# Kernel tuning notes

Measured on AMD Instinct MI355X. Metric: run time of the kernel, lower is better.

Reference implementation:

```python
import jax, jax.numpy as jnp
import numpy as np

B, T, S, H = 32, 512, 1024, 512


def setup_inputs() -> dict:
    key = jax.random.key(0)
    k1, k2, k3, k4, k5, k6 = jax.random.split(key, 6)
    scale = 1.0 / np.sqrt(H)
    return {
        "query": jax.random.normal(k1, (B, T, H), dtype=jnp.float32),
        "encoder_outputs": jax.random.normal(k2, (B, S, H), dtype=jnp.float32),
        "src_lengths": jax.random.randint(k3, (B,), 1, S + 1, dtype=jnp.int32),
        "Ws": jax.random.normal(k4, (H, H), dtype=jnp.float32) * scale,  # torch Linear weight [out,in]
        "Wh": jax.random.normal(k5, (H, H), dtype=jnp.float32) * scale,
        "v": jax.random.normal(k6, (H,), dtype=jnp.float32) * scale,
    }


def reference(query, encoder_outputs, src_lengths, Ws, Wh, v):
    # score(h_s, q_t) = v^T tanh(Wh h_s + Ws q_t); masked softmax over src; weighted sum.
    S_ = encoder_outputs.shape[1]
    # Wh(encoder_outputs) computed once (loop in original recomputes it each step; same math).
    Whe = jnp.einsum('bsh,oh->bso', encoder_outputs, Wh)  # [B,S,H]
    mask = jnp.arange(S_)[None, :] < src_lengths[:, None]  # [B,S] valid positions

    def step(carry, q_t):  # q_t: [B,H]
        Wsq = jnp.einsum('bh,oh->bo', q_t, Ws)            # [B,H]
        scores = jnp.einsum('bsh,h->bs', jnp.tanh(Whe + Wsq[:, None, :]), v)  # [B,S]
        scores = jnp.where(mask, scores, -jnp.inf)
        attn = jax.nn.softmax(scores, axis=-1)            # [B,S]
        ctx = jnp.einsum('bs,bsh->bh', attn, encoder_outputs)  # [B,H]
        return carry, (ctx, attn)

    _, (ctx_t, attn_t) = jax.lax.scan(step, None, jnp.swapaxes(query, 0, 1))
    context_vectors = jnp.swapaxes(ctx_t, 0, 1)  # [B,T,H]
    # original returns attention weights from the LAST timestep only
    return context_vectors, attn_t[-1]
```

## Files before the change

kernel.cpp:

```cpp
#include <hip/hip_runtime.h>


constexpr int B = 32, T = 512, S = 1024, H = 512;
constexpr int TT = 16;
constexpr int SP = S + 8;
constexpr float C2LOG2E = 2.88539008177792681f;

typedef float vf4 __attribute__((ext_vector_type(4)));
typedef float f32x4 __attribute__((ext_vector_type(4)));
typedef short bf16x8 __attribute__((ext_vector_type(8)));
typedef unsigned short ushort_t;

#define DEVI __device__ __forceinline__

DEVI unsigned pack_bf16(float a, float b) {
  unsigned ua = __builtin_bit_cast(unsigned, a) + 0x8000u;
  unsigned ub = __builtin_bit_cast(unsigned, b) + 0x8000u;
  return (ub & 0xffff0000u) | (ua >> 16);
}
DEVI ushort_t to_bf16u(float x) {
  return (ushort_t)((__builtin_bit_cast(unsigned, x) + 0x8000u) >> 16);
}
DEVI float bf_lo(unsigned d) { return __builtin_bit_cast(float, d << 16); }
DEVI float bf_hi(unsigned d) { return __builtin_bit_cast(float, d & 0xffff0000u); }
DEVI float bf_one(ushort_t u) { return __builtin_bit_cast(float, (unsigned)u << 16); }
DEVI float exp2c(float x) {
  return __builtin_amdgcn_exp2f(fminf(fmaxf(x, -15.f), 15.f));
}

constexpr int QBLK = (B * T / 128) * 4;
constexpr int EBLK = (B * S / 128) * 4;

__global__ __launch_bounds__(256)
void mfma_matmul_kernel(const float* __restrict__ query, const float* __restrict__ enc,
                        const float* __restrict__ Ws, const float* __restrict__ Wh,
                        float* __restrict__ q4, float* __restrict__ e4,
                        const int* __restrict__ lens) {
  __shared__ short As[128][72];
  __shared__ short Bs[128][72];
  const int tid = threadIdx.x;
  int blk = blockIdx.x;
  const bool isE = blk >= QBLK;
  if (isE) blk -= QBLK;
  const int bx = blk & 3, by = blk >> 2;
  const int row0 = by * 128, col0 = bx * 128;
  const float* A = isE ? enc : query;
  const float* W = isE ? Wh : Ws;
  if (isE && (row0 % S) >= lens[row0 / S]) return;

  const int lr = tid >> 4;
  const int lc = (tid & 15) * 4;
  const int lane = tid & 63, wv = tid >> 6;
  const int wm = (wv >> 1) * 64, wn = (wv & 1) * 64;
  const int lrow = lane & 15, lkg = (lane >> 4) * 8;

  f32x4 acc[4][4] = {};
  for (int k0 = 0; k0 < H; k0 += 64) {
    __syncthreads();
#pragma unroll
    for (int u = 0; u < 8; ++u) {
      int r = lr + u * 16;
      float4 av = *(const float4*)&A[(size_t)(row0 + r) * H + k0 + lc];
      *(uint2*)&As[r][lc] = make_uint2(pack_bf16(av.x, av.y), pack_bf16(av.z, av.w));
      float4 wv4 = *(const float4*)&W[(size_t)(col0 + r) * H + k0 + lc];
      *(uint2*)&Bs[r][lc] = make_uint2(pack_bf16(wv4.x, wv4.y), pack_bf16(wv4.z, wv4.w));
    }
    __syncthreads();
#pragma unroll
    for (int ks = 0; ks < 64; ks += 32) {
      bf16x8 af[4], bfr[4];
#pragma unroll
      for (int i = 0; i < 4; ++i) {
        af[i] = *(const bf16x8*)&As[wm + i * 16 + lrow][ks + lkg];
        bfr[i] = *(const bf16x8*)&Bs[wn + i * 16 + lrow][ks + lkg];
      }
#pragma unroll
      for (int mt = 0; mt < 4; ++mt)
#pragma unroll
        for (int nt = 0; nt < 4; ++nt)
          acc[mt][nt] = __builtin_amdgcn_mfma_f32_16x16x32_bf16(
              af[mt], bfr[nt], acc[mt][nt], 0, 0, 0);
    }
  }

  const int crow = (lane >> 4) * 4, ccol = lane & 15;
  if (!isE) {
    const int b = row0 / T;
#pragma unroll
    for (int mt = 0; mt < 4; ++mt) {
      const int m = (row0 % T) + wm + mt * 16 + crow;
      const int tile_t = m >> 2;
#pragma unroll
      for (int nt = 0; nt < 4; ++nt) {
        const int n = col0 + wn + nt * 16 + ccol;
        float* base = q4 + (size_t)b * T * H + (size_t)tile_t * (4 * H) +
                      (n >> 2) * 16 + (n & 3);
        f32x4 a = acc[mt][nt];
#pragma unroll
        for (int reg = 0; reg < 4; ++reg) base[reg * 4] = exp2c(C2LOG2E * a[reg]);
      }
    }
  } else {
    const int b = row0 / S;
#pragma unroll
    for (int mt = 0; mt < 4; ++mt) {
      const int s0 = (row0 % S) + wm + mt * 16 + crow;
#pragma unroll
      for (int nt = 0; nt < 4; ++nt) {
        const int n = col0 + wn + nt * 16 + ccol;
        float* base = e4 + (size_t)b * H * S + (size_t)(n >> 2) * (4 * S) +
                      (size_t)s0 * 4 + (n & 3);
        f32x4 a = acc[mt][nt];
#pragma unroll
        for (int reg = 0; reg < 4; ++reg) base[reg * 4] = exp2c(C2LOG2E * a[reg]);
      }
    }
  }
}

DEVI void tree4(float& acc, vf4 q, vf4 vv, vf4 e) {
  float a0 = __builtin_fmaf(q[0], e[0], 1.0f);
  float a1 = __builtin_fmaf(q[1], e[1], 1.0f);
  float a2 = __builtin_fmaf(q[2], e[2], 1.0f);
  float a3 = __builtin_fmaf(q[3], e[3], 1.0f);
  float d01 = a0 * a1, d23 = a2 * a3;
  float n01 = __builtin_fmaf(vv[1], a0, vv[0] * a1);
  float n23 = __builtin_fmaf(vv[3], a2, vv[2] * a3);
  float d = d01 * d23;
  float n = __builtin_fmaf(n23, d01, n01 * d23);
  acc = __builtin_fmaf(n, __builtin_amdgcn_rcpf(d), acc);
}

DEVI vf4 qload4(const ushort_t (&s_q4)[32][64], int h4q, int t) {
  uint2 qu = *(const uint2*)&s_q4[h4q][t * 4];
  vf4 q = {bf_lo(qu.x), bf_hi(qu.x), bf_lo(qu.y), bf_hi(qu.y)};
  return q;
}

DEVI void stage_quarter(ushort_t (&s_q4)[32][64], const vf4* __restrict__ qsrc,
                        int qt, int tid) {
  __syncthreads();
#pragma unroll
  for (int u = 0; u < 2; ++u) {
    int g = tid + u * 256;
    int tile = g >> 7, rem = g & 127;
    int h4q = rem >> 2, i = rem & 3;
    vf4 qv = qsrc[tile * 512 + (qt * 32 + h4q) * 4 + i];
    uint2 pk = make_uint2(pack_bf16(qv[0], qv[1]), pack_bf16(qv[2], qv[3]));
    ((uint2*)&s_q4[0][0])[h4q * 16 + tile * 4 + i] = pk;
  }
  __syncthreads();
}

template <int NSIM>
DEVI void passN16(ushort_t (&s_q4)[32][64], const vf4* __restrict__ qsrc,
                  const float* __restrict__ v, const float* __restrict__ e4b,
                  ushort_t (&s_sc16)[TT][SP], int wv, int lane) {
  const int tid = wv * 64 + lane;
  float acc[NSIM][TT];
#pragma unroll
  for (int r = 0; r < NSIM; ++r)
#pragma unroll
    for (int t = 0; t < TT; ++t) acc[r][t] = 0.f;
  const float* ep = e4b + (size_t)(wv * 64 + lane) * 4;
  for (int qt = 0; qt < 4; ++qt) {
    stage_quarter(s_q4, qsrc, qt, tid);
    for (int h4q = 0; h4q < 32; ++h4q) {
      const int h4 = qt * 32 + h4q;
      vf4 e[NSIM];
#pragma unroll
      for (int r = 0; r < NSIM; ++r)
        e[r] = *(const vf4*)(ep + (size_t)h4 * (S * 4) + r * 1024);
      vf4 vv = *(const vf4*)(v + h4 * 4);
#pragma unroll
      for (int t = 0; t < TT; ++t) {
        vf4 q = qload4(s_q4, h4q, t);
#pragma unroll
        for (int r = 0; r < NSIM; ++r) tree4(acc[r][t], q, vv, e[r]);
      }
    }
  }
#pragma unroll
  for (int r = 0; r < NSIM; ++r) {
    const int s = (wv + 4 * r) * 64 + lane;
#pragma unroll
    for (int t = 0; t < TT; ++t) s_sc16[t][s] = to_bf16u(-2.0f * acc[r][t]);
  }
}

template <int R>
DEVI void passTail16(ushort_t (&s_q4)[32][64], const vf4* __restrict__ qsrc,
                     const float* __restrict__ v, const float* __restrict__ e4b,
                     ushort_t (&s_sc16)[TT][SP], int kbase, int wv, int lane) {
  const int tid = wv * 64 + lane;
  float acc[R][4];
#pragma unroll
  for (int r = 0; r < R; ++r)
#pragma unroll
    for (int jj = 0; jj < 4; ++jj) acc[r][jj] = 0.f;
  const float* ep = e4b + (size_t)(kbase * 64 + lane) * 4;
  for (int qt = 0; qt < 4; ++qt) {
    stage_quarter(s_q4, qsrc, qt, tid);
    for (int h4q = 0; h4q < 32; ++h4q) {
      const int h4 = qt * 32 + h4q;
      vf4 vv = *(const vf4*)(v + h4 * 4);
      vf4 e[R];
#pragma unroll
      for (int r = 0; r < R; ++r)
        e[r] = *(const vf4*)(ep + (size_t)h4 * (S * 4) + r * 256);
#pragma unroll
      for (int jj = 0; jj < 4; ++jj) {
        vf4 q = qload4(s_q4, h4q, wv + 4 * jj);
#pragma unroll
        for (int r = 0; r < R; ++r) tree4(acc[r][jj], q, vv, e[r]);
      }
    }
  }
#pragma unroll
  for (int r = 0; r < R; ++r)
#pragma unroll
    for (int jj = 0; jj < 4; ++jj)
      s_sc16[wv + 4 * jj][(kbase + r) * 64 + lane] = to_bf16u(-2.0f * acc[r][jj]);
}

__global__ __launch_bounds__(256, 4)
void attn_fused_kernel(const float* __restrict__ wsq, const float* __restrict__ wheT,
                       const float* __restrict__ enc, const float* __restrict__ v,
                       const int* __restrict__ lens, float* __restrict__ out) {
  __shared__ __align__(16) ushort_t s_sc16[TT][SP];
  __shared__ __align__(16) ushort_t s_q4[32][64];
  __shared__ long long s_w[32];
  __shared__ int s_bsel;

  const int tid = threadIdx.x;
  const int xcd = blockIdx.x & 7;
  const int j = blockIdx.x >> 3;
  const int slot = j >> 5;
  const int tt = j & 31;

  if (tid < 32) s_w[tid] = ((long long)lens[tid] << 8) + tid;
  __syncthreads();
  if (tid < 32) {
    long long wb = s_w[tid];
    int rank = 0;
#pragma unroll
    for (int b2 = 0; b2 < 32; ++b2) rank += (s_w[b2] > wb);
    int myrank = slot * 8 + ((slot & 1) ? (7 - xcd) : xcd);
    if (rank == myrank) s_bsel = tid;
  }
  __syncthreads();
  const int b = __builtin_amdgcn_readfirstlane(s_bsel);
  const int len = lens[b];

  {
    const int wv = tid >> 6, lane = tid & 63;
    const int NS = (len + 63) >> 6;
    const int nsw = NS >> 2;
    const int R = NS & 3;
    const float* e4b = wheT + (size_t)b * H * S;
    const vf4* qsrc = (const vf4*)(wsq + (size_t)b * T * H + (size_t)tt * (TT * H));
    switch (nsw) {
      case 1: passN16<1>(s_q4, qsrc, v, e4b, s_sc16, wv, lane); break;
      case 2: passN16<2>(s_q4, qsrc, v, e4b, s_sc16, wv, lane); break;
      case 3: passN16<3>(s_q4, qsrc, v, e4b, s_sc16, wv, lane); break;
      case 4: passN16<4>(s_q4, qsrc, v, e4b, s_sc16, wv, lane); break;
      default: break;
    }
    switch (R) {
      case 1: passTail16<1>(s_q4, qsrc, v, e4b, s_sc16, nsw * 4, wv, lane); break;
      case 2: passTail16<2>(s_q4, qsrc, v, e4b, s_sc16, nsw * 4, wv, lane); break;
      case 3: passTail16<3>(s_q4, qsrc, v, e4b, s_sc16, nsw * 4, wv, lane); break;
      default: break;
    }
  }
  __syncthreads();

  {
    const int wv = tid >> 6, lane = tid & 63;
#pragma unroll
    for (int jj = 0; jj < 4; ++jj) {
      const int tr = wv + 4 * jj;
      float ps[S / 64];
      float sum = 0.f;
#pragma unroll
      for (int i = 0; i < S / 64; ++i) {
        int s = lane + 64 * i;
        float sc = bf_one(s_sc16[tr][s]);
        float p = (s < len) ? __builtin_amdgcn_exp2f(sc * 1.44269504088896341f) : 0.f;
        ps[i] = p;
        sum += p;
      }
#pragma unroll
      for (int o = 1; o < 64; o <<= 1) sum += __shfl_xor(sum, o, 64);
      float rs = 1.0f / sum;
#pragma unroll
      for (int i = 0; i < S / 64; ++i) {
        float pn = ps[i] * rs;
        s_sc16[tr][lane + 64 * i] = to_bf16u(pn);
        if (tt == T / TT - 1 && tr == TT - 1)
          out[(size_t)B * T * H + (size_t)b * S + lane + 64 * i] = pn;
      }
    }
  }
  __syncthreads();

  {
    const int wv = tid >> 6, lane = tid & 63;
    const int lrow = lane & 15, lkg = (lane >> 4) * 8;
    const int hbase = wv * 128;
    const float* encb = enc + (size_t)b * S * H;
    f32x4 acc[8] = {};
    const int nch = (len + 31) >> 5;
    for (int kc = 0; kc < nch; ++kc) {
      const int k0 = kc * 32 + lkg;
      bf16x8 pa = *(const bf16x8*)&s_sc16[lrow][k0];
#pragma unroll
      for (int nt = 0; nt < 8; ++nt) {
        const int h = hbase + nt * 16 + lrow;
        const float* ep = encb + (size_t)k0 * H + h;
        float b0 = ep[0 * H], b1 = ep[1 * H], b2 = ep[2 * H], b3 = ep[3 * H];
        float b4 = ep[4 * H], b5 = ep[5 * H], b6 = ep[6 * H], b7 = ep[7 * H];
        uint4 uu = make_uint4(pack_bf16(b0, b1), pack_bf16(b2, b3),
                              pack_bf16(b4, b5), pack_bf16(b6, b7));
        bf16x8 bfr = __builtin_bit_cast(bf16x8, uu);
        acc[nt] = __builtin_amdgcn_mfma_f32_16x16x32_bf16(pa, bfr, acc[nt], 0, 0, 0);
      }
    }
    const int crow = (lane >> 4) * 4, ccol = lane & 15;
#pragma unroll
    for (int nt = 0; nt < 8; ++nt) {
      const int h = hbase + nt * 16 + ccol;
#pragma unroll
      for (int reg = 0; reg < 4; ++reg) {
        const int t = crow + reg;
        out[((size_t)b * T + tt * TT + t) * H + h] = acc[nt][reg];
      }
    }
  }
}

extern "C" void kernel_launch(void* const* d_in, const int* in_sizes, int n_in,
                              void* d_out, int out_size, void* d_ws, size_t ws_size,
                              hipStream_t stream) {
  const float* query = (const float*)d_in[0];
  const float* enc   = (const float*)d_in[1];
  const int*   lens  = (const int*)d_in[2];
  const float* Ws    = (const float*)d_in[3];
  const float* Wh    = (const float*)d_in[4];
  const float* v     = (const float*)d_in[5];
  float* out = (float*)d_out;
  float* wsq  = (float*)d_ws;
  float* wheT = wsq + (size_t)B * T * H;

  mfma_matmul_kernel<<<dim3(QBLK + EBLK), 256, 0, stream>>>(query, enc, Ws, Wh, wsq, wheT, lens);
  attn_fused_kernel<<<dim3(B * (T / TT)), 256, 0, stream>>>(wsq, wheT, enc, v, lens, out);
}
```

Before: 496.2 us.

## Merge rational tanh sums over eight hidden dims and cap per-pass S chunks

The rational-form tanh score accumulation now combines eight hidden dimensions per reciprocal instead of four. This halves the rcp count and cuts the accumulator update work per element. The main S pass is split into chunks of at most two sub-tiles per call instead of one call with up to four, which lowers accumulator register pressure but restages Wsq in LDS once per chunk. The -2 scale is folded into the softmax exponent constant. Products of eight denominators risk overflow or precision loss in fp32.

```diff
diff --git a/kernel.cpp b/kernel.cpp
--- a/kernel.cpp
+++ b/kernel.cpp
@@ -118,17 +118,27 @@
   }
 }
 
-DEVI void tree4(float& acc, vf4 q, vf4 vv, vf4 e) {
-  float a0 = __builtin_fmaf(q[0], e[0], 1.0f);
-  float a1 = __builtin_fmaf(q[1], e[1], 1.0f);
-  float a2 = __builtin_fmaf(q[2], e[2], 1.0f);
-  float a3 = __builtin_fmaf(q[3], e[3], 1.0f);
-  float d01 = a0 * a1, d23 = a2 * a3;
-  float n01 = __builtin_fmaf(vv[1], a0, vv[0] * a1);
-  float n23 = __builtin_fmaf(vv[3], a2, vv[2] * a3);
-  float d = d01 * d23;
-  float n = __builtin_fmaf(n23, d01, n01 * d23);
-  acc = __builtin_fmaf(n, __builtin_amdgcn_rcpf(d), acc);
+DEVI void tree8(float& acc, vf4 qa, vf4 qb, vf4 va, vf4 vb, vf4 ea, vf4 eb) {
+  float a0 = __builtin_fmaf(qa[0], ea[0], 1.0f);
+  float a1 = __builtin_fmaf(qa[1], ea[1], 1.0f);
+  float a2 = __builtin_fmaf(qa[2], ea[2], 1.0f);
+  float a3 = __builtin_fmaf(qa[3], ea[3], 1.0f);
+  float b0 = __builtin_fmaf(qb[0], eb[0], 1.0f);
+  float b1 = __builtin_fmaf(qb[1], eb[1], 1.0f);
+  float b2 = __builtin_fmaf(qb[2], eb[2], 1.0f);
+  float b3 = __builtin_fmaf(qb[3], eb[3], 1.0f);
+  float dA01 = a0 * a1, dA23 = a2 * a3;
+  float dB01 = b0 * b1, dB23 = b2 * b3;
+  float nA01 = __builtin_fmaf(va[1], a0, va[0] * a1);
+  float nA23 = __builtin_fmaf(va[3], a2, va[2] * a3);
+  float nB01 = __builtin_fmaf(vb[1], b0, vb[0] * b1);
+  float nB23 = __builtin_fmaf(vb[3], b2, vb[2] * b3);
+  float dA = dA01 * dA23, dB = dB01 * dB23;
+  float nA = __builtin_fmaf(nA23, dA01, nA01 * dA23);
+  float nB = __builtin_fmaf(nB23, dB01, nB01 * dB23);
+  float D = dA * dB;
+  float N = __builtin_fmaf(nA, dB, nB * dA);
+  acc = __builtin_fmaf(N, __builtin_amdgcn_rcpf(D), acc);
 }
 
 DEVI vf4 qload4(const ushort_t (&s_q4)[32][64], int h4q, int t) {
@@ -155,36 +165,41 @@
 template <int NSIM>
 DEVI void passN16(ushort_t (&s_q4)[32][64], const vf4* __restrict__ qsrc,
                   const float* __restrict__ v, const float* __restrict__ e4b,
-                  ushort_t (&s_sc16)[TT][SP], int wv, int lane) {
+                  ushort_t (&s_sc16)[TT][SP], int ks0, int wv, int lane) {
   const int tid = wv * 64 + lane;
   float acc[NSIM][TT];
 #pragma unroll
   for (int r = 0; r < NSIM; ++r)
 #pragma unroll
     for (int t = 0; t < TT; ++t) acc[r][t] = 0.f;
-  const float* ep = e4b + (size_t)(wv * 64 + lane) * 4;
+  const float* ep = e4b + (size_t)(wv * 64 + lane) * 4 + (size_t)ks0 * 1024;
   for (int qt = 0; qt < 4; ++qt) {
     stage_quarter(s_q4, qsrc, qt, tid);
-    for (int h4q = 0; h4q < 32; ++h4q) {
-      const int h4 = qt * 32 + h4q;
-      vf4 e[NSIM];
-#pragma unroll
-      for (int r = 0; r < NSIM; ++r)
-        e[r] = *(const vf4*)(ep + (size_t)h4 * (S * 4) + r * 1024);
-      vf4 vv = *(const vf4*)(v + h4 * 4);
+    for (int g = 0; g < 16; ++g) {
+      const int h4 = qt * 32 + 2 * g;
+      vf4 ea[NSIM], eb[NSIM];
+#pragma unroll
+      for (int r = 0; r < NSIM; ++r) {
+        ea[r] = *(const vf4*)(ep + (size_t)h4 * (S * 4) + r * 1024);
+        eb[r] = *(const vf4*)(ep + (size_t)(h4 + 1) * (S * 4) + r * 1024);
+      }
+      vf4 va = *(const vf4*)(v + h4 * 4);
+      vf4 vb = *(const vf4*)(v + h4 * 4 + 4);
 #pragma unroll
       for (int t = 0; t < TT; ++t) {
-        vf4 q = qload4(s_q4, h4q, t);
-#pragma unroll
-        for (int r = 0; r < NSIM; ++r) tree4(acc[r][t], q, vv, e[r]);
+        vf4 qa = qload4(s_q4, 2 * g, t);
+        vf4 qb = qload4(s_q4, 2 * g + 1, t);
+#pragma unroll
+        for (int r = 0; r < NSIM; ++r)
+          tree8(acc[r][t], qa, qb, va, vb, ea[r], eb[r]);
       }
     }
   }
 #pragma unroll
   for (int r = 0; r < NSIM; ++r) {
-    const int s = (wv + 4 * r) * 64 + lane;
-#pragma unroll
-    for (int t = 0; t < TT; ++t) s_sc16[t][s] = to_bf16u(-2.0f * acc[r][t]);
+    const int s = (wv + 4 * (ks0 + r)) * 64 + lane;
+#pragma unroll
+    for (int t = 0; t < TT; ++t) s_sc16[t][s] = to_bf16u(acc[r][t]);
   }
 }
 
@@ -201,18 +216,23 @@
   const float* ep = e4b + (size_t)(kbase * 64 + lane) * 4;
   for (int qt = 0; qt < 4; ++qt) {
     stage_quarter(s_q4, qsrc, qt, tid);
-    for (int h4q = 0; h4q < 32; ++h4q) {
-      const int h4 = qt * 32 + h4q;
-      vf4 vv = *(const vf4*)(v + h4 * 4);
-      vf4 e[R];
-#pragma unroll
-      for (int r = 0; r < R; ++r)
-        e[r] = *(const vf4*)(ep + (size_t)h4 * (S * 4) + r * 256);
+    for (int g = 0; g < 16; ++g) {
+      const int h4 = qt * 32 + 2 * g;
+      vf4 va = *(const vf4*)(v + h4 * 4);
+      vf4 vb = *(const vf4*)(v + h4 * 4 + 4);
+      vf4 ea[R], eb[R];
+#pragma unroll
+      for (int r = 0; r < R; ++r) {
+        ea[r] = *(const vf4*)(ep + (size_t)h4 * (S * 4) + r * 256);
+        eb[r] = *(const vf4*)(ep + (size_t)(h4 + 1) * (S * 4) + r * 256);
+      }
 #pragma unroll
       for (int jj = 0; jj < 4; ++jj) {
-        vf4 q = qload4(s_q4, h4q, wv + 4 * jj);
-#pragma unroll
-        for (int r = 0; r < R; ++r) tree4(acc[r][jj], q, vv, e[r]);
+        vf4 qa = qload4(s_q4, 2 * g, wv + 4 * jj);
+        vf4 qb = qload4(s_q4, 2 * g + 1, wv + 4 * jj);
+#pragma unroll
+        for (int r = 0; r < R; ++r)
+          tree8(acc[r][jj], qa, qb, va, vb, ea[r], eb[r]);
       }
     }
   }
@@ -220,7 +240,7 @@
   for (int r = 0; r < R; ++r)
 #pragma unroll
     for (int jj = 0; jj < 4; ++jj)
-      s_sc16[wv + 4 * jj][(kbase + r) * 64 + lane] = to_bf16u(-2.0f * acc[r][jj]);
+      s_sc16[wv + 4 * jj][(kbase + r) * 64 + lane] = to_bf16u(acc[r][jj]);
 }
 
 __global__ __launch_bounds__(256, 4)
@@ -259,13 +279,11 @@
     const int R = NS & 3;
     const float* e4b = wheT + (size_t)b * H * S;
     const vf4* qsrc = (const vf4*)(wsq + (size_t)b * T * H + (size_t)tt * (TT * H));
-    switch (nsw) {
-      case 1: passN16<1>(s_q4, qsrc, v, e4b, s_sc16, wv, lane); break;
-      case 2: passN16<2>(s_q4, qsrc, v, e4b, s_sc16, wv, lane); break;
-      case 3: passN16<3>(s_q4, qsrc, v, e4b, s_sc16, wv, lane); break;
-      case 4: passN16<4>(s_q4, qsrc, v, e4b, s_sc16, wv, lane); break;
-      default: break;
-    }
+    int k0 = 0;
+    for (; k0 + 2 <= nsw; k0 += 2)
+      passN16<2>(s_q4, qsrc, v, e4b, s_sc16, k0, wv, lane);
+    if (k0 < nsw)
+      passN16<1>(s_q4, qsrc, v, e4b, s_sc16, k0, wv, lane);
     switch (R) {
       case 1: passTail16<1>(s_q4, qsrc, v, e4b, s_sc16, nsw * 4, wv, lane); break;
       case 2: passTail16<2>(s_q4, qsrc, v, e4b, s_sc16, nsw * 4, wv, lane); break;
@@ -286,7 +304,7 @@
       for (int i = 0; i < S / 64; ++i) {
         int s = lane + 64 * i;
         float sc = bf_one(s_sc16[tr][s]);
-        float p = (s < len) ? __builtin_amdgcn_exp2f(sc * 1.44269504088896341f) : 0.f;
+        float p = (s < len) ? __builtin_amdgcn_exp2f(sc * -C2LOG2E) : 0.f;
         ps[i] = p;
         sum += p;
       }
```

Result: no change. 502.7 us (+1.3%).
